# Kernel tuning notes

Measured on AMD Instinct MI355X. Metric: run time of the kernel, lower is better.

Reference implementation:

```python
import jax, jax.numpy as jnp
import numpy as np

BLOCK = 256          # block_size
K_IN = 64            # in_features // block_size
K_OUT = 64           # out_features // block_size
K_HALF = BLOCK // 2 + 1  # 129
INIT_SCALE = 0.1


def setup_inputs() -> dict:
    key = jax.random.key(0)
    kx, kr, ki = jax.random.split(key, 3)
    x = jax.random.normal(kx, (2048, K_IN * BLOCK), dtype=jnp.float32)
    W_real = jax.random.normal(kr, (K_OUT, K_IN, K_HALF), dtype=jnp.float32) * INIT_SCALE
    W_imag = jax.random.normal(ki, (K_OUT, K_IN, K_HALF), dtype=jnp.float32) * INIT_SCALE
    # match __init__: DC and Nyquist bins have zero imaginary part
    W_imag = W_imag.at[..., 0].set(0.0)
    W_imag = W_imag.at[..., -1].set(0.0)
    return {"x": x, "W_real": W_real, "W_imag": W_imag}


def _full_spectrum(W_real, W_imag):
    # Reconstruct full conjugate-symmetric spectrum per block: (k_out,k_in,BLOCK)
    H = (W_real + 1j * W_imag).astype(jnp.complex64)          # half spectrum (...,K_HALF)
    nyq = H[..., -1:].real.astype(jnp.complex64)              # real Nyquist bin (even BLOCK)
    return jnp.concatenate(
        [H[..., :-1], nyq, jnp.conj(H[..., 1:-1])[..., ::-1]], axis=-1
    )


def reference(x, W_real, W_imag):
    B = x.shape[0]
    x_blocks = x.reshape(B, K_IN, BLOCK)                      # (B, k_in, b)
    X_fft = jnp.fft.fft(x_blocks, axis=-1)                    # (B, k_in, b) complex64
    W_full = _full_spectrum(W_real, W_imag)                   # (k_out, k_in, b)
    # block-circulant matvec in frequency domain, accumulated over input blocks
    out_fft = jnp.einsum('bjf,ijf->bif', X_fft, jnp.conj(W_full))
    out = jnp.fft.ifft(out_fft, axis=-1).real                 # (B, k_out, b)
    return out.reshape(B, K_OUT * BLOCK).astype(x.dtype)
```

## Files before the change

kernel.cpp:

```cpp
#include <hip/hip_runtime.h>

#define BATCH 2048
#define KIN   64
#define KOUT  64
#define NPT   256
#define NF    129
#define FSTRIDE (BATCH * KIN)
#define XPLANE ((size_t)NF * FSTRIDE)
#define WPLANE (NF * KIN * KOUT)
#define NFP 133

#define WAVE_SYNC() __asm__ volatile("s_waitcnt lgkmcnt(0)" ::: "memory")

__device__ __forceinline__ int PHI(int i) { return i + (i >> 5); }

template<int SIGN>
__device__ __forceinline__ void fft256_r4(float2* A, float2* B, int lane) {
  float2* src = A;
  float2* dst = B;
  const float C = SIGN * (6.28318530717958647692f / 256.f);
#pragma unroll
  for (int st = 0; st < 4; ++st) {
    const int m  = 1 << (2 * st);
    const int t  = lane;
    const int jm = t & ~(m - 1);
    float2 s0 = src[PHI(t)];
    float2 s1 = src[PHI(t + 64)];
    float2 s2 = src[PHI(t + 128)];
    float2 s3 = src[PHI(t + 192)];
    float sw, cw;
    __sincosf(C * (float)jm, &sw, &cw);
    float c2 = cw * cw - sw * sw, s2w = 2.f * cw * sw;
    float c3 = c2 * cw - s2w * sw, s3w = c2 * sw + s2w * cw;
    float apcx = s0.x + s2.x, apcy = s0.y + s2.y;
    float amcx = s0.x - s2.x, amcy = s0.y - s2.y;
    float bpdx = s1.x + s3.x, bpdy = s1.y + s3.y;
    float bmdx = s1.x - s3.x, bmdy = s1.y - s3.y;
    float sbx = (SIGN < 0) ? bmdy : -bmdy;
    float sby = (SIGN < 0) ? -bmdx : bmdx;
    float t1x = amcx + sbx, t1y = amcy + sby;
    float t3x = amcx - sbx, t3y = amcy - sby;
    float t2x = apcx - bpdx, t2y = apcy - bpdy;
    const int base = t + 3 * jm;
    dst[PHI(base)]         = make_float2(apcx + bpdx, apcy + bpdy);
    dst[PHI(base + m)]     = make_float2(cw * t1x - sw * t1y, cw * t1y + sw * t1x);
    dst[PHI(base + 2 * m)] = make_float2(c2 * t2x - s2w * t2y, c2 * t2y + s2w * t2x);
    dst[PHI(base + 3 * m)] = make_float2(c3 * t3x - s3w * t3y, c3 * t3y + s3w * t3x);
    WAVE_SYNC();
    float2* tmp = src; src = dst; dst = tmp;
  }
}

__global__ __launch_bounds__(256) void k0_wtrans(const float* __restrict__ Wre,
                                                 const float* __restrict__ Wim,
                                                 float* __restrict__ Wtr,
                                                 float* __restrict__ Wti) {
  __shared__ float T[32][33];
  const int f0 = blockIdx.y * 32;
  const int d0 = blockIdx.x * 32;
  const int t  = threadIdx.x;
  const int a  = t & 31, g = t >> 5;
#pragma unroll
  for (int pl = 0; pl < 2; ++pl) {
    const float* src = pl ? Wim : Wre;
    float* dst = pl ? Wti : Wtr;
    if (pl) __syncthreads();
#pragma unroll
    for (int it = 0; it < 4; ++it) {
      int dl = g + it * 8;
      int d  = d0 + dl;
      int s  = (d & 63) * 64 + (d >> 6);
      int f  = f0 + a;
      if (f < NF) T[dl][a] = src[(size_t)s * NF + f];
    }
    __syncthreads();
#pragma unroll
    for (int it = 0; it < 4; ++it) {
      int fl = g + it * 8;
      int f  = f0 + fl;
      if (f < NF) dst[(size_t)f * (KIN * KOUT) + d0 + a] = T[a][fl];
    }
  }
}

__global__ __launch_bounds__(256) void k1_rfft(const float* __restrict__ x,
                                               float* __restrict__ Xtr,
                                               float* __restrict__ Xti) {
  __shared__ float2 fbuf[4][2][264];
  __shared__ float Sr[32 * NFP];
  __shared__ float Si[32 * NFP];
  const int wave = threadIdx.x >> 6, lane = threadIdx.x & 63;
  const int b = blockIdx.x >> 1, h = blockIdx.x & 1;
  float2* A  = fbuf[wave][0];
  float2* Bp = fbuf[wave][1];
#pragma unroll
  for (int rr = 0; rr < 8; ++rr) {
    const int jt  = rr * 4 + wave;
    const int idx = b * 64 + h * 32 + jt;
    float4 v = reinterpret_cast<const float4*>(x + (size_t)idx * NPT)[lane];
    A[PHI(4 * lane + 0)] = make_float2(v.x, 0.f);
    A[PHI(4 * lane + 1)] = make_float2(v.y, 0.f);
    A[PHI(4 * lane + 2)] = make_float2(v.z, 0.f);
    A[PHI(4 * lane + 3)] = make_float2(v.w, 0.f);
    WAVE_SYNC();
    fft256_r4<-1>(A, Bp, lane);
    float2 z0 = A[PHI(lane)];
    float2 z1 = A[PHI(lane + 64)];
    Sr[jt * NFP + lane]      = z0.x;  Si[jt * NFP + lane]      = z0.y;
    Sr[jt * NFP + lane + 64] = z1.x;  Si[jt * NFP + lane + 64] = z1.y;
    if (lane == 0) {
      float2 z2 = A[PHI(128)];
      Sr[jt * NFP + 128] = z2.x;  Si[jt * NFP + 128] = z2.y;
    }
    WAVE_SYNC();
  }
  __syncthreads();
  const int c = threadIdx.x & 31;
  const size_t baseidx = (size_t)b * 64 + h * 32 + c;
#pragma unroll
  for (int it = 0; it < 17; ++it) {
    int f = (threadIdx.x >> 5) + it * 8;
    if (f < NF) {
      Xtr[(size_t)f * FSTRIDE + baseidx] = Sr[c * NFP + f];
      Xti[(size_t)f * FSTRIDE + baseidx] = Si[c * NFP + f];
    }
  }
}

__global__ __launch_bounds__(256) void k2_cgemm(float* __restrict__ Xr,
                                                float* __restrict__ Xi,
                                                const float* __restrict__ Wtr,
                                                const float* __restrict__ Wti) {
  __shared__ __align__(16) float Xlr[64 * 68];
  __shared__ __align__(16) float Xli[64 * 68];
  __shared__ __align__(16) float Wlr[64 * 68];
  __shared__ __align__(16) float Wli[64 * 68];

  const int f  = blockIdx.y;
  const int b0 = blockIdx.x * 64;
  const int t  = threadIdx.x;
  const size_t xbase = (size_t)f * FSTRIDE + (size_t)b0 * 64;
  const float* wpr = Wtr + (size_t)f * (KIN * KOUT);
  const float* wpi = Wti + (size_t)f * (KIN * KOUT);

#pragma unroll
  for (int it = 0; it < 4; ++it) {
    int n4 = (it * 256 + t) * 4;
    int j = n4 >> 6, i0 = n4 & 63;
    float4 wr = *reinterpret_cast<const float4*>(wpr + n4);
    float4 wi = *reinterpret_cast<const float4*>(wpi + n4);
    *reinterpret_cast<float4*>(&Wlr[j * 68 + i0]) = wr;
    *reinterpret_cast<float4*>(&Wli[j * 68 + i0]) = wi;
  }
#pragma unroll
  for (int it = 0; it < 4; ++it) {
    int n4 = (it * 256 + t) * 4;
    int r = n4 >> 6, j0 = n4 & 63;
    float4 xr = *reinterpret_cast<const float4*>(Xr + xbase + n4);
    float4 xi = *reinterpret_cast<const float4*>(Xi + xbase + n4);
    Xlr[(j0 + 0) * 68 + r] = xr.x; Xlr[(j0 + 1) * 68 + r] = xr.y;
    Xlr[(j0 + 2) * 68 + r] = xr.z; Xlr[(j0 + 3) * 68 + r] = xr.w;
    Xli[(j0 + 0) * 68 + r] = xi.x; Xli[(j0 + 1) * 68 + r] = xi.y;
    Xli[(j0 + 2) * 68 + r] = xi.z; Xli[(j0 + 3) * 68 + r] = xi.w;
  }
  __syncthreads();

  const int tx = t & 15, ty = t >> 4;
  const int i0 = tx * 4, r0 = ty * 4;
  float aR[4][4] = {};
  float aI[4][4] = {};

#pragma unroll 4
  for (int j = 0; j < 64; ++j) {
    float4 xr = *reinterpret_cast<const float4*>(&Xlr[j * 68 + r0]);
    float4 xi = *reinterpret_cast<const float4*>(&Xli[j * 68 + r0]);
    float4 wr = *reinterpret_cast<const float4*>(&Wlr[j * 68 + i0]);
    float4 wi = *reinterpret_cast<const float4*>(&Wli[j * 68 + i0]);
    float xra[4] = {xr.x, xr.y, xr.z, xr.w};
    float xia[4] = {xi.x, xi.y, xi.z, xi.w};
    float wra[4] = {wr.x, wr.y, wr.z, wr.w};
    float wia[4] = {wi.x, wi.y, wi.z, wi.w};
#pragma unroll
    for (int a = 0; a < 4; ++a)
#pragma unroll
      for (int c = 0; c < 4; ++c) {
        aR[a][c] += xra[a] * wra[c] + xia[a] * wia[c];
        aI[a][c] += xia[a] * wra[c] - xra[a] * wia[c];
      }
  }

#pragma unroll
  for (int a = 0; a < 4; ++a) {
    size_t g = xbase + (size_t)(r0 + a) * 64 + i0;
    *reinterpret_cast<float4*>(&Xr[g]) = make_float4(aR[a][0], aR[a][1], aR[a][2], aR[a][3]);
    *reinterpret_cast<float4*>(&Xi[g]) = make_float4(aI[a][0], aI[a][1], aI[a][2], aI[a][3]);
  }
}

__global__ __launch_bounds__(256) void k3_irfft(const float* __restrict__ Or,
                                                const float* __restrict__ Oi,
                                                float* __restrict__ out) {
  __shared__ float2 fbuf[4][2][264];
  __shared__ float Sr[32 * NFP];
  __shared__ float Si[32 * NFP];
  const int wave = threadIdx.x >> 6, lane = threadIdx.x & 63;
  const int b = blockIdx.x >> 1, h = blockIdx.x & 1;
  const int c = threadIdx.x & 31;
  const size_t baseidx = (size_t)b * 64 + h * 32 + c;
#pragma unroll
  for (int it = 0; it < 17; ++it) {
    int f = (threadIdx.x >> 5) + it * 8;
    if (f < NF) {
      Sr[c * NFP + f] = Or[(size_t)f * FSTRIDE + baseidx];
      Si[c * NFP + f] = Oi[(size_t)f * FSTRIDE + baseidx];
    }
  }
  __syncthreads();
  float2* A  = fbuf[wave][0];
  float2* Bp = fbuf[wave][1];
#pragma unroll
  for (int rr = 0; rr < 8; ++rr) {
    const int it8 = rr * 4 + wave;
    float re0 = Sr[it8 * NFP + lane],      im0 = Si[it8 * NFP + lane];
    float re1 = Sr[it8 * NFP + lane + 64], im1 = Si[it8 * NFP + lane + 64];
    A[PHI(lane)]      = make_float2(re0, im0);
    A[PHI(lane + 64)] = make_float2(re1, im1);
    if (lane) A[PHI(256 - lane)] = make_float2(re0, -im0);
    A[PHI(192 - lane)] = make_float2(re1, -im1);
    if (lane == 0)
      A[PHI(128)] = make_float2(Sr[it8 * NFP + 128], Si[it8 * NFP + 128]);
    WAVE_SYNC();
    fft256_r4<1>(A, Bp, lane);
    const float s = 1.0f / 256.f;
    float4 o;
    o.x = A[PHI(4 * lane + 0)].x * s;
    o.y = A[PHI(4 * lane + 1)].x * s;
    o.z = A[PHI(4 * lane + 2)].x * s;
    o.w = A[PHI(4 * lane + 3)].x * s;
    const int idx = b * 64 + h * 32 + it8;
    reinterpret_cast<float4*>(out + (size_t)idx * NPT)[lane] = o;
    WAVE_SYNC();
  }
}

extern "C" void kernel_launch(void* const* d_in, const int* in_sizes, int n_in,
                              void* d_out, int out_size, void* d_ws, size_t ws_size,
                              hipStream_t stream) {
  const float* x   = (const float*)d_in[0];
  const float* Wre = (const float*)d_in[1];
  const float* Wim = (const float*)d_in[2];
  float* out = (float*)d_out;
  float* ws  = (float*)d_ws;

  float* Xr  = ws;
  float* Xi  = ws + XPLANE;
  float* Wtr = ws + 2 * XPLANE;
  float* Wti = Wtr + WPLANE;

  hipLaunchKernelGGL(k0_wtrans, dim3(128, 5), dim3(256), 0, stream,
                     Wre, Wim, Wtr, Wti);
  hipLaunchKernelGGL(k1_rfft, dim3(BATCH * 2), dim3(256), 0, stream,
                     x, Xr, Xi);
  hipLaunchKernelGGL(k2_cgemm, dim3(BATCH / 64, NF), dim3(256), 0, stream,
                     Xr, Xi, Wtr, Wti);
  hipLaunchKernelGGL(k3_irfft, dim3(BATCH * 2), dim3(256), 0, stream,
                     Xr, Xi, out);
}
```

Before: 459.0 us.

## Pack two real FFTs per complex FFT and hoist twiddle computation

The forward transform now packs two real input rows into one complex 256-point FFT and separates the two spectra with conjugate-symmetry arithmetic. The inverse transform likewise combines two Hermitian spectra into one complex IFFT and writes the real and imaginary parts as two output rows. This halves the number of FFTs in both the rfft and irfft kernels. Twiddle factors are computed once per thread before the loop instead of once per stage per FFT, which costs extra registers. The complex GEMM stage is unchanged and likely dominates, so the end-to-end effect may be limited.

```diff
diff --git a/kernel.cpp b/kernel.cpp
--- a/kernel.cpp
+++ b/kernel.cpp
@@ -15,10 +15,31 @@
 __device__ __forceinline__ int PHI(int i) { return i + (i >> 5); }
 
 template<int SIGN>
-__device__ __forceinline__ void fft256_r4(float2* A, float2* B, int lane) {
+__device__ __forceinline__ void make_twiddles(int lane,
+                                              float (&cw)[4],  float (&sw)[4],
+                                              float (&c2w)[4], float (&s2w)[4],
+                                              float (&c3w)[4], float (&s3w)[4]) {
+  const float C = SIGN * (6.28318530717958647692f / 256.f);
+#pragma unroll
+  for (int st = 0; st < 4; ++st) {
+    const int m  = 1 << (2 * st);
+    const int jm = lane & ~(m - 1);
+    float s, c;
+    __sincosf(C * (float)jm, &s, &c);
+    cw[st] = c;  sw[st] = s;
+    c2w[st] = c * c - s * s;           s2w[st] = 2.f * c * s;
+    c3w[st] = c2w[st] * c - s2w[st] * s;
+    s3w[st] = c2w[st] * s + s2w[st] * c;
+  }
+}
+
+template<int SIGN>
+__device__ __forceinline__ void fft256_tw(float2* A, float2* B, int lane,
+                                          const float (&cw)[4],  const float (&sw)[4],
+                                          const float (&c2w)[4], const float (&s2w)[4],
+                                          const float (&c3w)[4], const float (&s3w)[4]) {
   float2* src = A;
   float2* dst = B;
-  const float C = SIGN * (6.28318530717958647692f / 256.f);
 #pragma unroll
   for (int st = 0; st < 4; ++st) {
     const int m  = 1 << (2 * st);
@@ -28,10 +49,6 @@
     float2 s1 = src[PHI(t + 64)];
     float2 s2 = src[PHI(t + 128)];
     float2 s3 = src[PHI(t + 192)];
-    float sw, cw;
-    __sincosf(C * (float)jm, &sw, &cw);
-    float c2 = cw * cw - sw * sw, s2w = 2.f * cw * sw;
-    float c3 = c2 * cw - s2w * sw, s3w = c2 * sw + s2w * cw;
     float apcx = s0.x + s2.x, apcy = s0.y + s2.y;
     float amcx = s0.x - s2.x, amcy = s0.y - s2.y;
     float bpdx = s1.x + s3.x, bpdy = s1.y + s3.y;
@@ -43,9 +60,12 @@
     float t2x = apcx - bpdx, t2y = apcy - bpdy;
     const int base = t + 3 * jm;
     dst[PHI(base)]         = make_float2(apcx + bpdx, apcy + bpdy);
-    dst[PHI(base + m)]     = make_float2(cw * t1x - sw * t1y, cw * t1y + sw * t1x);
-    dst[PHI(base + 2 * m)] = make_float2(c2 * t2x - s2w * t2y, c2 * t2y + s2w * t2x);
-    dst[PHI(base + 3 * m)] = make_float2(c3 * t3x - s3w * t3y, c3 * t3y + s3w * t3x);
+    dst[PHI(base + m)]     = make_float2(cw[st] * t1x - sw[st] * t1y,
+                                         cw[st] * t1y + sw[st] * t1x);
+    dst[PHI(base + 2 * m)] = make_float2(c2w[st] * t2x - s2w[st] * t2y,
+                                         c2w[st] * t2y + s2w[st] * t2x);
+    dst[PHI(base + 3 * m)] = make_float2(c3w[st] * t3x - s3w[st] * t3y,
+                                         c3w[st] * t3y + s3w[st] * t3x);
     WAVE_SYNC();
     float2* tmp = src; src = dst; dst = tmp;
   }
@@ -93,24 +113,39 @@
   const int b = blockIdx.x >> 1, h = blockIdx.x & 1;
   float2* A  = fbuf[wave][0];
   float2* Bp = fbuf[wave][1];
-#pragma unroll
-  for (int rr = 0; rr < 8; ++rr) {
-    const int jt  = rr * 4 + wave;
-    const int idx = b * 64 + h * 32 + jt;
-    float4 v = reinterpret_cast<const float4*>(x + (size_t)idx * NPT)[lane];
-    A[PHI(4 * lane + 0)] = make_float2(v.x, 0.f);
-    A[PHI(4 * lane + 1)] = make_float2(v.y, 0.f);
-    A[PHI(4 * lane + 2)] = make_float2(v.z, 0.f);
-    A[PHI(4 * lane + 3)] = make_float2(v.w, 0.f);
-    WAVE_SYNC();
-    fft256_r4<-1>(A, Bp, lane);
-    float2 z0 = A[PHI(lane)];
-    float2 z1 = A[PHI(lane + 64)];
-    Sr[jt * NFP + lane]      = z0.x;  Si[jt * NFP + lane]      = z0.y;
-    Sr[jt * NFP + lane + 64] = z1.x;  Si[jt * NFP + lane + 64] = z1.y;
+
+  float cw[4], sw[4], c2w[4], s2w[4], c3w[4], s3w[4];
+  make_twiddles<-1>(lane, cw, sw, c2w, s2w, c3w, s3w);
+
+#pragma unroll
+  for (int u = 0; u < 4; ++u) {
+    const int p   = u * 4 + wave;
+    const int jt1 = 2 * p, jt2 = 2 * p + 1;
+    const size_t idx1 = (size_t)b * 64 + h * 32 + jt1;
+    float4 va = reinterpret_cast<const float4*>(x + idx1 * NPT)[lane];
+    float4 vb = reinterpret_cast<const float4*>(x + (idx1 + 1) * NPT)[lane];
+    A[PHI(4 * lane + 0)] = make_float2(va.x, vb.x);
+    A[PHI(4 * lane + 1)] = make_float2(va.y, vb.y);
+    A[PHI(4 * lane + 2)] = make_float2(va.z, vb.z);
+    A[PHI(4 * lane + 3)] = make_float2(va.w, vb.w);
+    WAVE_SYNC();
+    fft256_tw<-1>(A, Bp, lane, cw, sw, c2w, s2w, c3w, s3w);
+    float2 zf  = A[PHI(lane)];
+    float2 zfm = A[PHI((256 - lane) & 255)];
+    float2 zg  = A[PHI(lane + 64)];
+    float2 zgm = A[PHI(192 - lane)];
+    Sr[jt1 * NFP + lane] = 0.5f * (zf.x + zfm.x);
+    Si[jt1 * NFP + lane] = 0.5f * (zf.y - zfm.y);
+    Sr[jt2 * NFP + lane] = 0.5f * (zf.y + zfm.y);
+    Si[jt2 * NFP + lane] = 0.5f * (zfm.x - zf.x);
+    Sr[jt1 * NFP + lane + 64] = 0.5f * (zg.x + zgm.x);
+    Si[jt1 * NFP + lane + 64] = 0.5f * (zg.y - zgm.y);
+    Sr[jt2 * NFP + lane + 64] = 0.5f * (zg.y + zgm.y);
+    Si[jt2 * NFP + lane + 64] = 0.5f * (zgm.x - zg.x);
     if (lane == 0) {
-      float2 z2 = A[PHI(128)];
-      Sr[jt * NFP + 128] = z2.x;  Si[jt * NFP + 128] = z2.y;
+      float2 zn = A[PHI(128)];
+      Sr[jt1 * NFP + 128] = zn.x;  Si[jt1 * NFP + 128] = 0.f;
+      Sr[jt2 * NFP + 128] = zn.y;  Si[jt2 * NFP + 128] = 0.f;
     }
     WAVE_SYNC();
   }
@@ -218,27 +253,40 @@
   __syncthreads();
   float2* A  = fbuf[wave][0];
   float2* Bp = fbuf[wave][1];
-#pragma unroll
-  for (int rr = 0; rr < 8; ++rr) {
-    const int it8 = rr * 4 + wave;
-    float re0 = Sr[it8 * NFP + lane],      im0 = Si[it8 * NFP + lane];
-    float re1 = Sr[it8 * NFP + lane + 64], im1 = Si[it8 * NFP + lane + 64];
-    A[PHI(lane)]      = make_float2(re0, im0);
-    A[PHI(lane + 64)] = make_float2(re1, im1);
-    if (lane) A[PHI(256 - lane)] = make_float2(re0, -im0);
-    A[PHI(192 - lane)] = make_float2(re1, -im1);
-    if (lane == 0)
-      A[PHI(128)] = make_float2(Sr[it8 * NFP + 128], Si[it8 * NFP + 128]);
-    WAVE_SYNC();
-    fft256_r4<1>(A, Bp, lane);
+
+  float cw[4], sw[4], c2w[4], s2w[4], c3w[4], s3w[4];
+  make_twiddles<1>(lane, cw, sw, c2w, s2w, c3w, s3w);
+
+#pragma unroll
+  for (int u = 0; u < 4; ++u) {
+    const int p  = u * 4 + wave;
+    const int p1 = 2 * p, p2 = 2 * p + 1;
+    float a1r = Sr[p1 * NFP + lane],      a1i = Si[p1 * NFP + lane];
+    float b1r = Sr[p1 * NFP + lane + 64], b1i = Si[p1 * NFP + lane + 64];
+    float a2r = Sr[p2 * NFP + lane],      a2i = Si[p2 * NFP + lane];
+    float b2r = Sr[p2 * NFP + lane + 64], b2i = Si[p2 * NFP + lane + 64];
+    A[PHI(lane)]      = make_float2(a1r - a2i, a1i + a2r);
+    A[PHI(lane + 64)] = make_float2(b1r - b2i, b1i + b2r);
+    if (lane) A[PHI(256 - lane)] = make_float2(a1r + a2i, a2r - a1i);
+    A[PHI(192 - lane)] = make_float2(b1r + b2i, b2r - b1i);
+    if (lane == 0) {
+      float n1r = Sr[p1 * NFP + 128], n1i = Si[p1 * NFP + 128];
+      float n2r = Sr[p2 * NFP + 128], n2i = Si[p2 * NFP + 128];
+      A[PHI(128)] = make_float2(n1r - n2i, n1i + n2r);
+    }
+    WAVE_SYNC();
+    fft256_tw<1>(A, Bp, lane, cw, sw, c2w, s2w, c3w, s3w);
     const float s = 1.0f / 256.f;
-    float4 o;
-    o.x = A[PHI(4 * lane + 0)].x * s;
-    o.y = A[PHI(4 * lane + 1)].x * s;
-    o.z = A[PHI(4 * lane + 2)].x * s;
-    o.w = A[PHI(4 * lane + 3)].x * s;
-    const int idx = b * 64 + h * 32 + it8;
-    reinterpret_cast<float4*>(out + (size_t)idx * NPT)[lane] = o;
+    float4 o1, o2;
+    float2 e0 = A[PHI(4 * lane + 0)];
+    float2 e1 = A[PHI(4 * lane + 1)];
+    float2 e2 = A[PHI(4 * lane + 2)];
+    float2 e3 = A[PHI(4 * lane + 3)];
+    o1.x = e0.x * s; o1.y = e1.x * s; o1.z = e2.x * s; o1.w = e3.x * s;
+    o2.x = e0.y * s; o2.y = e1.y * s; o2.z = e2.y * s; o2.w = e3.y * s;
+    const size_t idx1 = (size_t)b * 64 + h * 32 + p1;
+    reinterpret_cast<float4*>(out + idx1 * NPT)[lane] = o1;
+    reinterpret_cast<float4*>(out + (idx1 + 1) * NPT)[lane] = o2;
     WAVE_SYNC();
   }
 }
```

After: 426.7 us. 1.08x faster.
